# Optimization experiments

Hardware: AMD Instinct MI355X
Metric: run time of the kernel (lower is better)

The kernel has to match this reference:

```python
import jax, jax.numpy as jnp
import numpy as np

N_NODES = 100000
N_EDGES = 3200000
C, H, F = 512, 256, 64


def spmm(edge_row, edge_col, edge_val, Z):
    # (A @ Z)[i] = sum over edges e with row[e]==i of val[e] * Z[col[e]]
    msgs = edge_val[:, None] * Z[edge_col]  # [E, d]
    return jax.ops.segment_sum(msgs, edge_row, num_segments=N_NODES)


def setup_inputs() -> dict:
    key = jax.random.key(0)
    k1, k2, k3, k4, k5, k6, k7 = jax.random.split(key, 7)
    X = jax.random.normal(k1, (N_NODES, C), dtype=jnp.float32)
    edge_row = jax.random.randint(k2, (N_EDGES,), 0, N_NODES, dtype=jnp.int32)
    edge_col = jax.random.randint(k3, (N_EDGES,), 0, N_NODES, dtype=jnp.int32)
    edge_val = jax.random.uniform(k4, (N_EDGES,), dtype=jnp.float32)
    W0 = jax.random.normal(k5, (C, H), dtype=jnp.float32) * (C ** -0.5)
    Wh1 = jax.random.normal(k6, (H, H), dtype=jnp.float32) * (H ** -0.5)
    W1 = jax.random.normal(k7, (H, F), dtype=jnp.float32) * (H ** -0.5)
    return {"X": X, "edge_row": edge_row, "edge_col": edge_col,
            "edge_val": edge_val, "W0": W0, "Wh1": Wh1, "W1": W1}


def reference(X, edge_row, edge_col, edge_val, W0, Wh1, W1):
    # layer 0: relu(A @ (X W0))   (dropout=0 -> identity)
    Z = jax.nn.relu(spmm(edge_row, edge_col, edge_val, X @ W0))
    # hidden layers (num_layers - 2 = 1)
    Z = jax.nn.relu(spmm(edge_row, edge_col, edge_val, Z @ Wh1))
    # output layer: softmax(A @ (Z W1), axis=-1)
    Z = jax.nn.softmax(spmm(edge_row, edge_col, edge_val, Z @ W1), axis=-1)
    return Z
```

## Files before the change

### kernel.cpp

```cpp
#include <hip/hip_runtime.h>
#include <cstdint>
#include <cstddef>


#define SCAN_B 1024

typedef __attribute__((ext_vector_type(8))) short short8_t;
typedef __attribute__((ext_vector_type(4))) short short4_t;
typedef __attribute__((ext_vector_type(4))) float f32x4;

__device__ __forceinline__ short bf16_hi(float x) {
    union { float f; unsigned u; } c; c.f = x;
    return (short)(c.u >> 16);
}
__device__ __forceinline__ float bf16_f32(short h) {
    union { float f; unsigned u; } c; c.u = ((unsigned)(unsigned short)h) << 16;
    return c.f;
}

__device__ __forceinline__ void gload_lds16(const void* g, void* l) {
    __builtin_amdgcn_global_load_lds(
        (const __attribute__((address_space(1))) void*)g,
        (__attribute__((address_space(3))) void*)l, 16, 0, 0);
}

#define GBAR() asm volatile("s_barrier" ::: "memory")
#define LGKM0() asm volatile("s_waitcnt lgkmcnt(0)" ::: "memory")

__device__ __forceinline__ void wait_vm(int n) {
    switch (n) {
        case 0:  asm volatile("s_waitcnt vmcnt(0)"  ::: "memory"); break;
        case 6:  asm volatile("s_waitcnt vmcnt(6)"  ::: "memory"); break;
        case 8:  asm volatile("s_waitcnt vmcnt(8)"  ::: "memory"); break;
        default: asm volatile("s_waitcnt vmcnt(10)" ::: "memory"); break;
    }
}


__global__ void count_rows_k(const int* __restrict__ row, int* __restrict__ deg, int E) {
    int e = blockIdx.x * blockDim.x + threadIdx.x;
    if (e < E) atomicAdd(&deg[row[e]], 1);
}

__global__ __launch_bounds__(SCAN_B) void scan1_k(const int* __restrict__ deg,
                                                  int* __restrict__ part,
                                                  int* __restrict__ bsum, int n) {
    __shared__ int buf[SCAN_B];
    int tid = threadIdx.x;
    int i = blockIdx.x * SCAN_B + tid;
    int v = (i < n) ? ((deg[i] + 3) & ~3) : 0;
    buf[tid] = v;
    __syncthreads();
    for (int off = 1; off < SCAN_B; off <<= 1) {
        int y = (tid >= off) ? buf[tid - off] : 0;
        __syncthreads();
        buf[tid] += y;
        __syncthreads();
    }
    if (i < n) part[i] = buf[tid] - v;
    if (tid == SCAN_B - 1) bsum[blockIdx.x] = buf[tid];
}

__global__ __launch_bounds__(128) void scan2_k(int* __restrict__ bsum, int nb) {
    __shared__ int buf[128];
    int tid = threadIdx.x;
    int v = (tid < nb) ? bsum[tid] : 0;
    buf[tid] = v;
    __syncthreads();
    for (int off = 1; off < 128; off <<= 1) {
        int y = (tid >= off) ? buf[tid - off] : 0;
        __syncthreads();
        buf[tid] += y;
        __syncthreads();
    }
    if (tid < nb) bsum[tid] = buf[tid] - v;
    if (tid == nb - 1) bsum[nb] = buf[tid];
}

__global__ __launch_bounds__(SCAN_B) void scan3_k(int* __restrict__ rowptr,
                                                  const int* __restrict__ bsum,
                                                  int* __restrict__ cursor, int n, int nb) {
    int i = blockIdx.x * SCAN_B + threadIdx.x;
    if (i < n) {
        int v = rowptr[i] + bsum[blockIdx.x];
        rowptr[i] = v;
        cursor[i] = v;
    }
    if (i == 0) rowptr[n] = bsum[nb];
}

__global__ __launch_bounds__(256) void scatter_xcd_k(const int* __restrict__ row,
                                                     const int* __restrict__ col,
                                                     const float* __restrict__ val,
                                                     int* __restrict__ cursor,
                                                     int2* __restrict__ ecv,
                                                     int E, int gsz) {
    const int g = blockIdx.x & 7;
    const int rank = blockIdx.x >> 3;
    const int R = gridDim.x >> 3;
    const int lo = g * gsz, hi = lo + gsz;
    for (int e = rank * 256 + threadIdx.x; e < E; e += R * 256) {
        int r = row[e];
        if (r >= lo && r < hi) {
            int p = atomicAdd(&cursor[r], 1);
            ecv[p] = make_int2(col[e], __float_as_int(val[e]));
        }
    }
}


__global__ void split_w_k(const float* __restrict__ W, short* __restrict__ Bhl,
                          int K, int M) {
    int i = blockIdx.x * 256 + threadIdx.x;
    if (i >= K * M) return;
    int k = i / M, m = i - k * M;
    float x = W[i];
    short hi = bf16_hi(x);
    float r = x - bf16_f32(hi);
    short lo = bf16_hi(r);
    int g = k >> 3, j = k & 7;
    Bhl[(size_t)m * (2 * K) + 16 * g + j] = hi;
    Bhl[(size_t)m * (2 * K) + 16 * g + 8 + j] = lo;
}


template <int K, int BN, int NWR, int NWC, bool AF32>
__global__ __launch_bounds__(256) void gemm_hl(const void* __restrict__ Av,
                                               const short* __restrict__ Bhl,
                                               short* __restrict__ ZQ,
                                               float* __restrict__ scl, int N) {
    constexpr int BM = 64 * NWR;
    constexpr int NF = BN / NWC / 16;
    constexpr int NT = K / 32;
    constexpr int LB = BN / 8 / 4;
    constexpr int LA = AF32 ? 0 : BM / 8 / 4;
    constexpr int L  = LA + LB;
    __shared__ short Ald[2][BM * 64];
    __shared__ short Bld[2][BN * 64];

    const int tid = threadIdx.x, lane = tid & 63, w = tid >> 6;
    const int wr = w / NWC, wc = w % NWC;
    const int row0 = blockIdx.x * BM;
    const int l8 = lane >> 3;
    const int sx = (lane & 7) ^ l8;

    const short* Ahl = (const short*)Av;
    const float* Af  = (const float*)Av;
    const int arow = tid >> 2, aq = tid & 3;
    const int akey = arow & 7;

    f32x4 acc[4][NF] = {};

    auto stageB = [&](int t, int b) {
#pragma unroll
        for (int ch = w; ch < BN / 8; ch += 4)
            gload_lds16(Bhl + (size_t)(ch * 8 + l8) * (2 * K) + (size_t)t * 64 + sx * 8,
                        &Bld[b][ch * 512]);
    };
    auto stageAg = [&](int t, int b) {
#pragma unroll
        for (int ch = w; ch < BM / 8; ch += 4)
            gload_lds16(Ahl + (size_t)(row0 + ch * 8 + l8) * (2 * K) + (size_t)t * 64 + sx * 8,
                        &Ald[b][ch * 512]);
    };
    auto loadAf = [&](int t, float4& x0, float4& x1) {
        int gr = row0 + arow;
        x0 = make_float4(0.f, 0.f, 0.f, 0.f); x1 = x0;
        if (gr < N) {
            x0 = *(const float4*)&Af[(size_t)gr * K + t * 32 + aq * 8];
            x1 = *(const float4*)&Af[(size_t)gr * K + t * 32 + aq * 8 + 4];
        }
    };
    auto writeAf = [&](int b, float4 x0, float4 x1) {
        float f[8] = {x0.x, x0.y, x0.z, x0.w, x1.x, x1.y, x1.z, x1.w};
        short8_t hi, lo;
#pragma unroll
        for (int j = 0; j < 8; ++j) {
            short hh = bf16_hi(f[j]);
            hi[j] = hh;
            lo[j] = bf16_hi(f[j] - bf16_f32(hh));
        }
        *(short8_t*)&Ald[b][arow * 64 + ((2 * aq) ^ akey) * 8] = hi;
        *(short8_t*)&Ald[b][arow * 64 + ((2 * aq + 1) ^ akey) * 8] = lo;
    };

    float4 pxa[2], pxb[2];
    if constexpr (AF32) {
        float4 a0, a1, b0, b1;
        loadAf(0, a0, a1); stageB(0, 0); writeAf(0, a0, a1);
        loadAf(1, b0, b1); stageB(1, 1); writeAf(1, b0, b1);
        loadAf(2, pxa[0], pxb[0]);
        wait_vm(10);
        LGKM0();
    } else {
        stageAg(0, 0); stageB(0, 0);
        stageAg(1, 1); stageB(1, 1);
        wait_vm(L);
    }
    GBAR();

#pragma unroll
    for (int t = 0; t < NT; ++t) {
        const int cur = t & 1;

        const int sH = (lane >> 4) * 2, sL2 = sH + 1;
        short8_t ah[4], al[4];
#pragma unroll
        for (int m = 0; m < 4; ++m) {
            int rl = wr * 64 + m * 16 + (lane & 15);
            int key = rl & 7;
            ah[m] = *(const short8_t*)&Ald[cur][rl * 64 + (sH ^ key) * 8];
            al[m] = *(const short8_t*)&Ald[cur][rl * 64 + (sL2 ^ key) * 8];
        }
#pragma unroll
        for (int n = 0; n < NF; ++n) {
            int cl = wc * (BN / NWC) + n * 16 + (lane & 15);
            int key = cl & 7;
            short8_t bh = *(const short8_t*)&Bld[cur][cl * 64 + (sH ^ key) * 8];
            short8_t bl = *(const short8_t*)&Bld[cur][cl * 64 + (sL2 ^ key) * 8];
#pragma unroll
            for (int m = 0; m < 4; ++m) {
                acc[m][n] = __builtin_amdgcn_mfma_f32_16x16x32_bf16(ah[m], bh, acc[m][n], 0, 0, 0);
                acc[m][n] = __builtin_amdgcn_mfma_f32_16x16x32_bf16(ah[m], bl, acc[m][n], 0, 0, 0);
                acc[m][n] = __builtin_amdgcn_mfma_f32_16x16x32_bf16(al[m], bh, acc[m][n], 0, 0, 0);
            }
        }

        GBAR();
        if constexpr (AF32) {
            if (t + 3 < NT) loadAf(t + 3, pxa[(t + 1) & 1], pxb[(t + 1) & 1]);
            if (t + 2 < NT) {
                stageB(t + 2, cur);
                writeAf(cur, pxa[t & 1], pxb[t & 1]);
            }
            LGKM0();
            wait_vm((t + 3 < NT ? 2 : 0) + (t + 2 < NT ? LB : 0));
        } else {
            if (t + 2 < NT) { stageAg(t + 2, cur); stageB(t + 2, cur); }
            wait_vm(t + 2 < NT ? L : 0);
        }
        GBAR();
    }

    const int lg = lane >> 4, lc = lane & 15;
    float* maxb = (float*)&Ald[0][0];
    float rmax[4][4];
#pragma unroll
    for (int m = 0; m < 4; ++m)
#pragma unroll
        for (int r = 0; r < 4; ++r) {
            float v = 0.f;
#pragma unroll
            for (int n = 0; n < NF; ++n) v = fmaxf(v, fabsf(acc[m][n][r]));
#pragma unroll
            for (int o = 8; o >= 1; o >>= 1) v = fmaxf(v, __shfl_xor(v, o));
            rmax[m][r] = v;
        }
    if constexpr (NWC > 1) {
        __syncthreads();
        if (lc == 0)
#pragma unroll
            for (int m = 0; m < 4; ++m)
#pragma unroll
                for (int r = 0; r < 4; ++r)
                    maxb[(wr * 64 + m * 16 + lg * 4 + r) * NWC + wc] = rmax[m][r];
        __syncthreads();
    }
#pragma unroll
    for (int m = 0; m < 4; ++m)
#pragma unroll
        for (int r = 0; r < 4; ++r) {
            int rl = wr * 64 + m * 16 + lg * 4 + r;
            float v = rmax[m][r];
            if constexpr (NWC > 1) {
                v = maxb[rl * NWC];
#pragma unroll
                for (int q = 1; q < NWC; ++q) v = fmaxf(v, maxb[rl * NWC + q]);
            }
            int grow = row0 + rl;
            if (grow < N) {
                float inv = (v > 0.f) ? 32767.f / v : 0.f;
                if (lc == 0 && wc == 0) scl[grow] = v * (1.f / 32767.f);
#pragma unroll
                for (int n = 0; n < NF; ++n)
                    ZQ[(size_t)grow * BN + wc * (BN / NWC) + n * 16 + lc] =
                        (short)rintf(acc[m][n][r] * inv);
            }
        }
}


__global__ __launch_bounds__(256) void spmm_agg256_k(const int* __restrict__ rowptr,
                                                     const int2* __restrict__ ecv,
                                                     const short* __restrict__ Q,
                                                     const float* __restrict__ scl,
                                                     short* __restrict__ Zhl, int N) {
    int row = blockIdx.x * 4 + (threadIdx.x >> 6);
    if (row >= N) return;
    const int lane = threadIdx.x & 63;
    const int half = lane >> 5;
    const int l32 = lane & 31;
    int s = rowptr[row], e = rowptr[row + 1];
    const short8_t* Qv = (const short8_t*)Q;
    f32x4 a0 = {0.f, 0.f, 0.f, 0.f}, a1 = a0;
    for (int i = s; i < e; i += 4) {
        int4 A = *(const int4*)(ecv + i);
        int4 B = *(const int4*)(ecv + i + 2);
        int   cA = half ? A.z : A.x;
        float wA = __int_as_float(half ? A.w : A.y) * scl[cA];
        int   cB = half ? B.z : B.x;
        float wB = __int_as_float(half ? B.w : B.y) * scl[cB];
        short8_t qA = Qv[(size_t)cA * 32 + l32];
        short8_t qB = Qv[(size_t)cB * 32 + l32];
#pragma unroll
        for (int j = 0; j < 4; ++j) {
            a0[j] = fmaf(wA, (float)qA[j], a0[j]);
            a1[j] = fmaf(wA, (float)qA[j + 4], a1[j]);
            a0[j] = fmaf(wB, (float)qB[j], a0[j]);
            a1[j] = fmaf(wB, (float)qB[j + 4], a1[j]);
        }
    }
#pragma unroll
    for (int j = 0; j < 4; ++j) {
        a0[j] += __shfl_xor(a0[j], 32);
        a1[j] += __shfl_xor(a1[j], 32);
    }
    if (half == 0) {
        short8_t hi, lo;
#pragma unroll
        for (int j = 0; j < 4; ++j) {
            float r0 = fmaxf(a0[j], 0.f), r1 = fmaxf(a1[j], 0.f);
            short h0 = bf16_hi(r0), h1 = bf16_hi(r1);
            hi[j] = h0; hi[j + 4] = h1;
            lo[j] = bf16_hi(r0 - bf16_f32(h0));
            lo[j + 4] = bf16_hi(r1 - bf16_f32(h1));
        }
        size_t base = (size_t)row * 512 + l32 * 16;
        *(short8_t*)&Zhl[base] = hi;
        *(short8_t*)&Zhl[base + 8] = lo;
    }
}

__global__ __launch_bounds__(256) void spmm_softmax64_k(const int* __restrict__ rowptr,
                                                        const int2* __restrict__ ecv,
                                                        const short* __restrict__ Q,
                                                        const float* __restrict__ scl,
                                                        float* __restrict__ out, int N) {
    int row = blockIdx.x * 4 + (threadIdx.x >> 6);
    if (row >= N) return;
    const int lane = threadIdx.x & 63;
    const int q = lane >> 4;
    const int l16 = lane & 15;
    int s = rowptr[row], e = rowptr[row + 1];
    const short4_t* Qv = (const short4_t*)Q;
    f32x4 acc = {0.f, 0.f, 0.f, 0.f};
    for (int i = s; i < e; i += 4) {
        int4 A = *(const int4*)(ecv + i);
        int4 B = *(const int4*)(ecv + i + 2);
        int c = (q & 2) ? ((q & 1) ? B.z : B.x) : ((q & 1) ? A.z : A.x);
        int wbits = (q & 2) ? ((q & 1) ? B.w : B.y) : ((q & 1) ? A.w : A.y);
        float wv = __int_as_float(wbits) * scl[c];
        short4_t z = Qv[(size_t)c * 16 + l16];
#pragma unroll
        for (int j = 0; j < 4; ++j) acc[j] = fmaf(wv, (float)z[j], acc[j]);
    }
#pragma unroll
    for (int j = 0; j < 4; ++j) {
        acc[j] += __shfl_xor(acc[j], 16);
        acc[j] += __shfl_xor(acc[j], 32);
    }
    float m = fmaxf(fmaxf(acc[0], acc[1]), fmaxf(acc[2], acc[3]));
#pragma unroll
    for (int o = 8; o >= 1; o >>= 1) m = fmaxf(m, __shfl_xor(m, o));
    float p0 = __expf(acc[0] - m), p1 = __expf(acc[1] - m);
    float p2 = __expf(acc[2] - m), p3 = __expf(acc[3] - m);
    float ssum = p0 + p1 + p2 + p3;
#pragma unroll
    for (int o = 8; o >= 1; o >>= 1) ssum += __shfl_xor(ssum, o);
    if (q == 0) {
        float inv = 1.f / ssum;
        float4 o4 = make_float4(p0 * inv, p1 * inv, p2 * inv, p3 * inv);
        *(float4*)&out[(size_t)row * 64 + l16 * 4] = o4;
    }
}


extern "C" void kernel_launch(void* const* d_in, const int* in_sizes, int n_in,
                              void* d_out, int out_size, void* d_ws, size_t ws_size,
                              hipStream_t stream) {
    const float* X        = (const float*)d_in[0];
    const int*   edge_row = (const int*)d_in[1];
    const int*   edge_col = (const int*)d_in[2];
    const float* edge_val = (const float*)d_in[3];
    const float* W0       = (const float*)d_in[4];
    const float* Wh1      = (const float*)d_in[5];
    const float* W1       = (const float*)d_in[6];

    const int C = 512, H = 256, F = 64;
    const int N = in_sizes[0] / C;
    const int E = in_sizes[1];
    const int EPAD = E + 4 * N + 64;

    size_t off = 0;
    auto alloc = [&](size_t bytes) -> void* {
        void* p = (char*)d_ws + off;
        off += (bytes + 255) & ~(size_t)255;
        return p;
    };
    short* Zhl    = (short*)alloc((size_t)N * 2 * H * sizeof(short));
    short* ZQ     = (short*)alloc((size_t)N * H * sizeof(short));
    float* scl    = (float*)alloc((size_t)N * sizeof(float));
    int*   deg    = (int*)alloc((size_t)N * sizeof(int));
    int*   rowptr = (int*)alloc((size_t)(N + 1) * sizeof(int));
    int*   cursor = (int*)alloc((size_t)N * sizeof(int));
    int*   bsum   = (int*)alloc(129 * sizeof(int));
    int2*  ecv    = (int2*)alloc((size_t)EPAD * sizeof(int2));
    short* Bhl0   = (short*)alloc((size_t)H * 2 * C * sizeof(short));
    short* Bhl1   = (short*)alloc((size_t)H * 2 * H * sizeof(short));
    short* Bhl2   = (short*)alloc((size_t)F * 2 * H * sizeof(short));
    (void)ws_size;

    hipMemsetAsync(deg, 0, (size_t)N * sizeof(int), stream);
    hipMemsetAsync(ecv, 0, (size_t)EPAD * sizeof(int2), stream);
    count_rows_k<<<(E + 255) / 256, 256, 0, stream>>>(edge_row, deg, E);
    int nb = (N + SCAN_B - 1) / SCAN_B;
    scan1_k<<<nb, SCAN_B, 0, stream>>>(deg, rowptr, bsum, N);
    scan2_k<<<1, 128, 0, stream>>>(bsum, nb);
    scan3_k<<<nb, SCAN_B, 0, stream>>>(rowptr, bsum, cursor, N, nb);
    const int gsz = (N + 7) / 8;
    scatter_xcd_k<<<8 * 256, 256, 0, stream>>>(edge_row, edge_col, edge_val,
                                               cursor, ecv, E, gsz);

    split_w_k<<<(C * H + 255) / 256, 256, 0, stream>>>(W0, Bhl0, C, H);
    split_w_k<<<(H * H + 255) / 256, 256, 0, stream>>>(Wh1, Bhl1, H, H);
    split_w_k<<<(H * F + 255) / 256, 256, 0, stream>>>(W1, Bhl2, H, F);

    const int g64  = (N + 63) / 64;
    const int g128 = (N + 127) / 128;
    const int rg   = (N + 3) / 4;

    gemm_hl<512, 256, 1, 4, true><<<g64, 256, 0, stream>>>(X, Bhl0, ZQ, scl, N);
    spmm_agg256_k<<<rg, 256, 0, stream>>>(rowptr, ecv, ZQ, scl, Zhl, N);
    gemm_hl<256, 256, 1, 4, false><<<g64, 256, 0, stream>>>(Zhl, Bhl1, ZQ, scl, N);
    spmm_agg256_k<<<rg, 256, 0, stream>>>(rowptr, ecv, ZQ, scl, Zhl, N);
    gemm_hl<256, 64, 2, 2, false><<<g128, 256, 0, stream>>>(Zhl, Bhl2, ZQ, scl, N);
    spmm_softmax64_k<<<rg, 256, 0, stream>>>(rowptr, ecv, ZQ, scl,
                                             (float*)d_out, N);
}
```

Measured before the change: 1.122 ms.

## Vectorize edge counting/scatter loads and restructure GEMM A-prefetch pipeline

count_rows_k becomes a grid-stride kernel with 2048 blocks that reads row indices as int4 and issues four atomics per load. scatter_xcd_k reads eight row indices per iteration through two int4 loads. In the gemm_hl kernel, the fp32 A-tile prefetch distance drops from 3 to 2 stages, the loads move to the top of each iteration, and the loop unroll is reduced to 2, which lowers register pressure at the cost of less latency hiding. The wait_vm counts are retuned to match the new number of outstanding loads.

```diff
diff --git a/kernel.cpp b/kernel.cpp
--- a/kernel.cpp
+++ b/kernel.cpp
@@ -37,9 +37,19 @@
 }
 
 
-__global__ void count_rows_k(const int* __restrict__ row, int* __restrict__ deg, int E) {
-    int e = blockIdx.x * blockDim.x + threadIdx.x;
-    if (e < E) atomicAdd(&deg[row[e]], 1);
+__global__ __launch_bounds__(256) void count_rows_k(const int* __restrict__ row,
+                                                    int* __restrict__ deg, int E) {
+    const int tidg = blockIdx.x * 256 + threadIdx.x;
+    const int T = gridDim.x * 256;
+    const int E4 = E >> 2;
+    for (int c = tidg; c < E4; c += T) {
+        int4 r = *(const int4*)&row[c * 4];
+        atomicAdd(&deg[r.x], 1);
+        atomicAdd(&deg[r.y], 1);
+        atomicAdd(&deg[r.z], 1);
+        atomicAdd(&deg[r.w], 1);
+    }
+    for (int e = E4 * 4 + tidg; e < E; e += T) atomicAdd(&deg[row[e]], 1);
 }
 
 __global__ __launch_bounds__(SCAN_B) void scan1_k(const int* __restrict__ deg,
@@ -96,10 +106,24 @@
                                                      int2* __restrict__ ecv,
                                                      int E, int gsz) {
     const int g = blockIdx.x & 7;
-    const int rank = blockIdx.x >> 3;
-    const int R = gridDim.x >> 3;
     const int lo = g * gsz, hi = lo + gsz;
-    for (int e = rank * 256 + threadIdx.x; e < E; e += R * 256) {
+    const int tidg = (blockIdx.x >> 3) * 256 + threadIdx.x;
+    const int T = (gridDim.x >> 3) * 256;
+    const int E8 = E >> 3;
+    for (int c = tidg; c < E8; c += T) {
+        const int e = c * 8;
+        int4 r0 = *(const int4*)&row[e];
+        int4 r1 = *(const int4*)&row[e + 4];
+        int rr[8] = {r0.x, r0.y, r0.z, r0.w, r1.x, r1.y, r1.z, r1.w};
+#pragma unroll
+        for (int j = 0; j < 8; ++j) {
+            if (rr[j] >= lo && rr[j] < hi) {
+                int p = atomicAdd(&cursor[rr[j]], 1);
+                ecv[p] = make_int2(col[e + j], __float_as_int(val[e + j]));
+            }
+        }
+    }
+    for (int e = E8 * 8 + tidg; e < E; e += T) {
         int r = row[e];
         if (r >= lo && r < hi) {
             int p = atomicAdd(&cursor[r], 1);
@@ -184,14 +208,12 @@
         *(short8_t*)&Ald[b][arow * 64 + ((2 * aq + 1) ^ akey) * 8] = lo;
     };
 
-    float4 pxa[2], pxb[2];
     if constexpr (AF32) {
-        float4 a0, a1, b0, b1;
-        loadAf(0, a0, a1); stageB(0, 0); writeAf(0, a0, a1);
-        loadAf(1, b0, b1); stageB(1, 1); writeAf(1, b0, b1);
-        loadAf(2, pxa[0], pxb[0]);
-        wait_vm(10);
+        float4 a0, a1;
+        loadAf(0, a0, a1); writeAf(0, a0, a1); stageB(0, 0);
+        loadAf(1, a0, a1); writeAf(1, a0, a1); stageB(1, 1);
         LGKM0();
+        wait_vm(8);
     } else {
         stageAg(0, 0); stageB(0, 0);
         stageAg(1, 1); stageB(1, 1);
@@ -199,9 +221,14 @@
     }
     GBAR();
 
-#pragma unroll
+#pragma unroll 2
     for (int t = 0; t < NT; ++t) {
         const int cur = t & 1;
+
+        float4 px0, px1;
+        if constexpr (AF32) {
+            if (t + 2 < NT) loadAf(t + 2, px0, px1);
+        }
 
         const int sH = (lane >> 4) * 2, sL2 = sH + 1;
         short8_t ah[4], al[4];
@@ -228,13 +255,12 @@
 
         GBAR();
         if constexpr (AF32) {
-            if (t + 3 < NT) loadAf(t + 3, pxa[(t + 1) & 1], pxb[(t + 1) & 1]);
             if (t + 2 < NT) {
+                writeAf(cur, px0, px1);
                 stageB(t + 2, cur);
-                writeAf(cur, pxa[t & 1], pxb[t & 1]);
             }
             LGKM0();
-            wait_vm((t + 3 < NT ? 2 : 0) + (t + 2 < NT ? LB : 0));
+            wait_vm(t + 2 < NT ? 8 : 0);
         } else {
             if (t + 2 < NT) { stageAg(t + 2, cur); stageB(t + 2, cur); }
             wait_vm(t + 2 < NT ? L : 0);
@@ -422,7 +448,7 @@
 
     hipMemsetAsync(deg, 0, (size_t)N * sizeof(int), stream);
     hipMemsetAsync(ecv, 0, (size_t)EPAD * sizeof(int2), stream);
-    count_rows_k<<<(E + 255) / 256, 256, 0, stream>>>(edge_row, deg, E);
+    count_rows_k<<<2048, 256, 0, stream>>>(edge_row, deg, E);
     int nb = (N + SCAN_B - 1) / SCAN_B;
     scan1_k<<<nb, SCAN_B, 0, stream>>>(deg, rowptr, bsum, N);
     scan2_k<<<1, 128, 0, stream>>>(bsum, nb);
```

Result: no change. 1.132 ms (+0.8%).
